# Kernel optimization log

Hardware: AMD Instinct MI355X
Metric: run time of the kernel (lower is better)

## Reference

```python
import jax, jax.numpy as jnp
import numpy as np

K = 3
Q = 4
NSF = 16
C2 = NSF * 2  # 32 channels in each multi-scale volume


def _x_shift():
    # Faithful replication of the torch init (note Python floor division: -3//2 == -2)
    grid = np.linspace(-K // 2, K // 2, K)  # [-2.0, -0.5, 1.0]
    g3 = np.stack(np.meshgrid(grid, grid, grid), axis=0).transpose(2, 1, 3, 0)
    return jnp.asarray(g3.reshape(-1, 3), dtype=jnp.float32)  # [27, 3]


def trilinear_sample(vol, coords):
    # vol: [C, D, H, W]; coords: [P, 3], normalized order (x->W, y->H, z->D)
    # matches F.grid_sample(mode='bilinear', padding_mode='border', align_corners=True)
    C, D, H, W = vol.shape
    def to_pix(c, size):
        return jnp.clip((c + 1.0) * 0.5 * (size - 1), 0.0, float(size - 1))
    ix = to_pix(coords[:, 0], W)
    iy = to_pix(coords[:, 1], H)
    iz = to_pix(coords[:, 2], D)
    x0f, y0f, z0f = jnp.floor(ix), jnp.floor(iy), jnp.floor(iz)
    x0 = x0f.astype(jnp.int32); y0 = y0f.astype(jnp.int32); z0 = z0f.astype(jnp.int32)
    x1 = jnp.minimum(x0 + 1, W - 1)
    y1 = jnp.minimum(y0 + 1, H - 1)
    z1 = jnp.minimum(z0 + 1, D - 1)
    fx, fy, fz = ix - x0f, iy - y0f, iz - z0f
    def g(zi, yi, xi):
        return vol[:, zi, yi, xi]  # [C, P]
    out = (g(z0, y0, x0) * ((1 - fz) * (1 - fy) * (1 - fx))
         + g(z0, y0, x1) * ((1 - fz) * (1 - fy) * fx)
         + g(z0, y1, x0) * ((1 - fz) * fy * (1 - fx))
         + g(z0, y1, x1) * ((1 - fz) * fy * fx)
         + g(z1, y0, x0) * (fz * (1 - fy) * (1 - fx))
         + g(z1, y0, x1) * (fz * (1 - fy) * fx)
         + g(z1, y1, x0) * (fz * fy * (1 - fx))
         + g(z1, y1, x1) * (fz * fy * fx))
    return out  # [C, P]


def _leaky(a):
    return jnp.where(a >= 0, a, 0.2 * a)


def reference(t, x, vol0, vol1, vol2, vol3, conv_w, conv_b, lfc_w, lfc_b,
              fc1_w, fc1_b, fc2_w, fc2_b, fc3_w, fc3_b, fc4_w, fc4_b):
    vols = [vol0, vol1, vol2, vol3]
    D1, D2, D3 = vol0.shape[2], vol0.shape[3], vol0.shape[4]
    Dm = max(D1, D2, D3)
    rescale = jnp.array([D3 / Dm, D2 / Dm, D1 / Dm], dtype=x.dtype)
    xs = _x_shift()
    m = x.shape[1]
    pts = x[0]  # [m, 3]
    cubes = jnp.zeros((C2, m * K * K * K), dtype=x.dtype)
    for q in range(Q):
        xq = pts[:, None, :] + xs * (2.0 * (2 ** q) / Dm)  # [m, 27, 3]
        xq = (xq / rescale).reshape(-1, 3)                  # [m*27, 3]
        cubes = cubes + trilinear_sample(vols[q][0], xq)    # sum over scales
    # torch wraps sampling in no_grad
    cubes = jax.lax.stop_gradient(cubes)
    # (C2, m, 27) -> (m, C2*27), matching view/permute/view in torch
    cubes = cubes.reshape(C2, m, K * K * K).transpose(1, 0, 2).reshape(m, C2 * K * K * K)
    # conv3d with kernel == cube -> per-point GEMM
    z_local = cubes @ conv_w.reshape(conv_w.shape[0], -1).T + conv_b   # [m, 64]
    z_local = z_local @ lfc_w.T + lfc_b                                 # [m, 128]
    z_point = _leaky(pts @ fc1_w.T + fc1_b)                             # [m, 128]
    z = jnp.concatenate([z_point, z_local], axis=-1)                    # [m, 256]
    z = _leaky(z @ fc2_w.T + fc2_b)                                     # [m, 512]
    z = _leaky(z @ fc3_w.T + fc3_b)                                     # [m, 256]
    dx = z @ fc4_w.T + fc4_b                                            # [m, 3]
    return dx[None]  # [1, m, 3]


def setup_inputs() -> dict:
    key = jax.random.key(0)
    ks = jax.random.split(key, 24)
    m, Dv, s = 50000, 64, 0.05
    inp = {
        't': jax.random.uniform(ks[0], (1,), dtype=jnp.float32),
        'x': jax.random.uniform(ks[1], (1, m, 3), dtype=jnp.float32),
    }
    for q in range(Q):
        inp[f'vol{q}'] = jax.random.normal(ks[2 + q], (1, C2, Dv, Dv, Dv), dtype=jnp.float32)
    inp['conv_w'] = jax.random.normal(ks[6], (NSF * 4, C2, K, K, K), dtype=jnp.float32) * s
    inp['conv_b'] = jax.random.normal(ks[7], (NSF * 4,), dtype=jnp.float32) * s
    inp['lfc_w'] = jax.random.normal(ks[8], (NSF * 8, NSF * 4), dtype=jnp.float32) * s
    inp['lfc_b'] = jax.random.normal(ks[9], (NSF * 8,), dtype=jnp.float32) * s
    inp['fc1_w'] = jax.random.normal(ks[10], (NSF * 8, 3), dtype=jnp.float32) * s
    inp['fc1_b'] = jax.random.normal(ks[11], (NSF * 8,), dtype=jnp.float32) * s
    inp['fc2_w'] = jax.random.normal(ks[12], (NSF * 32, NSF * 16), dtype=jnp.float32) * s
    inp['fc2_b'] = jax.random.normal(ks[13], (NSF * 32,), dtype=jnp.float32) * s
    inp['fc3_w'] = jax.random.normal(ks[14], (NSF * 16, NSF * 32), dtype=jnp.float32) * s
    inp['fc3_b'] = jax.random.normal(ks[15], (NSF * 16,), dtype=jnp.float32) * s
    inp['fc4_w'] = jax.random.normal(ks[16], (3, NSF * 16), dtype=jnp.float32) * s
    inp['fc4_b'] = jax.random.normal(ks[17], (3,), dtype=jnp.float32) * s
    return inp
```

## Files before the change

kernel.cpp:

```cpp
#include <hip/hip_runtime.h>
#include <hip/hip_bf16.h>

typedef __attribute__((ext_vector_type(8))) short short8;
typedef __attribute__((ext_vector_type(4))) float f32x4;
typedef __attribute__((ext_vector_type(2))) float f32x2;
typedef __attribute__((ext_vector_type(4))) int int32x4;

__device__ unsigned int llvm_amdgcn_raw_buffer_load_u32(int32x4 srsrc, int voffset,
                                                        int soffset, int aux)
    __asm("llvm.amdgcn.raw.buffer.load.i32");

#define VOXELS 262144
#define ZC_PAD 264
#define Z0_PAD 72
#define Z2_PAD 520
#define Z3_PAD 264
#define NCELL  512

template <bool VT16>
__global__ void k_transpose(const float* __restrict__ v0, const float* __restrict__ v1,
                            const float* __restrict__ v2, const float* __restrict__ v3,
                            void* __restrict__ vtp) {
    int b  = blockIdx.x;
    int q  = b >> 12;
    int zy = b & 4095;
    const float* src = (q == 0) ? v0 : (q == 1) ? v1 : (q == 2) ? v2 : v3;
    __shared__ float buf[32][65];
    int t = threadIdx.x;
    int x = t & 63, c0 = t >> 6;
    for (int cp = 0; cp < 32; cp += 4) {
        int c = c0 + cp;
        buf[c][x] = src[(size_t)c * VOXELS + (size_t)zy * 64 + x];
    }
    __syncthreads();
    int c = t & 31, xg = t >> 5;
    const size_t base = ((size_t)q * VOXELS + (size_t)zy * 64) * 32;
    for (int xx = xg; xx < 64; xx += 8) {
        if (VT16) ((__hip_bfloat16*)vtp)[base + xx * 32 + c] = __float2bfloat16(buf[c][xx]);
        else      ((float*)vtp)[base + xx * 32 + c] = buf[c][xx];
    }
}

__device__ __forceinline__ void prep_one(const float* __restrict__ W,
                                         __hip_bfloat16* __restrict__ wf,
                                         int K, int mode, int n) {
    int e = n & 7, lane = (n >> 3) & 63;
    int rest = n >> 9;
    int ksteps = K >> 5;
    int kstep = rest % ksteps, otile = rest / ksteps;
    int o = otile * 16 + (lane & 15);
    int k = kstep * 32 + (lane >> 4) * 8 + e;
    float v;
    if (mode == 1)      v = W[(size_t)o * K + (k & 31) * 27 + (k >> 5)];
    else if (mode == 2) v = (o < 3) ? W[(size_t)o * K + k] : 0.f;
    else                v = W[(size_t)o * K + k];
    wf[n] = __float2bfloat16(v);
}

__global__ void k_prepw_all(const float* __restrict__ conv_w, const float* __restrict__ lfc_w,
                            const float* __restrict__ fc2_w, const float* __restrict__ fc3_w,
                            const float* __restrict__ fc4_w,
                            __hip_bfloat16* __restrict__ w0f, __hip_bfloat16* __restrict__ w1f,
                            __hip_bfloat16* __restrict__ w2f, __hip_bfloat16* __restrict__ w3f,
                            __hip_bfloat16* __restrict__ w4f) {
    int n = blockIdx.x * blockDim.x + threadIdx.x;
    if (n < 55296)                prep_one(conv_w, w0f, 864, 1, n);
    else if (n < 63488)           prep_one(lfc_w,  w1f, 64,  0, n - 55296);
    else if (n < 194560)          prep_one(fc2_w,  w2f, 256, 0, n - 63488);
    else if (n < 325632)          prep_one(fc3_w,  w3f, 512, 0, n - 194560);
    else if (n < 329728)          prep_one(fc4_w,  w4f, 256, 2, n - 325632);
}

__device__ __forceinline__ int point_cell(float px, float py, float pz) {
    int cx = min(63, max(0, (int)(px * 31.5f + 31.5f))) >> 3;
    int cy = min(63, max(0, (int)(py * 31.5f + 31.5f))) >> 3;
    int cz = min(63, max(0, (int)(pz * 31.5f + 31.5f))) >> 3;
    int k = 0;
#pragma unroll
    for (int b = 0; b < 3; ++b)
        k |= (((cx >> b) & 1) << (3 * b)) | (((cy >> b) & 1) << (3 * b + 1))
           | (((cz >> b) & 1) << (3 * b + 2));
    return k;
}

__global__ void k_hist(const float* __restrict__ xin, int* __restrict__ hist, int m) {
    int p = blockIdx.x * blockDim.x + threadIdx.x;
    if (p >= m) return;
    atomicAdd(&hist[point_cell(xin[p * 3], xin[p * 3 + 1], xin[p * 3 + 2])], 1);
}

__global__ __launch_bounds__(64)
void k_scan(const int* __restrict__ hist, int* __restrict__ cursor) {
    const int t = threadIdx.x;
    int vals[8];
    int s = 0;
#pragma unroll
    for (int k = 0; k < 8; ++k) { vals[k] = hist[t * 8 + k]; s += vals[k]; }
    int pre = s;
#pragma unroll
    for (int off = 1; off < 64; off <<= 1) {
        int u = __shfl_up(pre, off);
        if (t >= off) pre += u;
    }
    int run = pre - s;
#pragma unroll
    for (int k = 0; k < 8; ++k) { cursor[t * 8 + k] = run; run += vals[k]; }
}

__global__ void k_scatter(const float* __restrict__ xin, int* __restrict__ cursor,
                          int* __restrict__ perm, int m) {
    int p = blockIdx.x * blockDim.x + threadIdx.x;
    if (p >= m) return;
    int cell = point_cell(xin[p * 3], xin[p * 3 + 1], xin[p * 3 + 2]);
    int pos = atomicAdd(&cursor[cell], 1);
    perm[pos] = p;
}

template <bool VT16, bool SORT>
__global__ __launch_bounds__(256, 4)
void k_sample(const float* __restrict__ xin, const void* __restrict__ vtp,
              const int* __restrict__ perm,
              __hip_bfloat16* __restrict__ fbuf, int m, int nblk) {
    __shared__ __align__(16) __hip_bfloat16 rowbuf[4][896];

    int b = blockIdx.x;
    {
        const int qd = nblk >> 3, r = nblk & 7;
        const int xcd = b & 7, i = b >> 3;
        b = (xcd < r) ? xcd * (qd + 1) + i : r * (qd + 1) + (xcd - r) * qd + i;
    }
    const int lane = threadIdx.x & 63;
    const int wv   = threadIdx.x >> 6;
    const int sp = b * 4 + wv;
    if (sp >= m) return;
    const int p = SORT ? perm[sp] : sp;

    const float px = xin[p * 3 + 0];
    const float py = xin[p * 3 + 1];
    const float pz = xin[p * 3 + 2];

    const int pr  = lane & 15;
    const int cxb = (lane >> 4) & 1;
    const int cyb = (lane >> 5) & 1;

    const float pxs = px * 31.5f + 31.5f;
    const float pys = py * 31.5f + 31.5f;
    const float pzs = pz * 31.5f + 31.5f;

    const int XS  = VT16 ? 6 : 7;
    const int YS  = VT16 ? 12 : 13;
    const int ZS  = VT16 ? 18 : 19;
    const int QS  = VT16 ? 24 : 25;
    const int PRB = VT16 ? 4 : 8;

    int   xoS[4][3], yoS[4][3], zoS[4][3], zdS[4][3];
    float wxS[4][3], wyS[4][3], wzS[4][3];
#pragma unroll
    for (int q = 0; q < 4; ++q) {
        const float sc31 = (float)(2 << q) * (31.5f / 64.0f);
#pragma unroll
        for (int pos = 0; pos < 3; ++pos) {
            const float gv = (-2.0f + 1.5f * (float)pos) * sc31;
            {
                float ix = fminf(fmaxf(pxs + gv, 0.f), 63.f);
                float xf = floorf(ix); int x0 = (int)xf; float fx = ix - xf;
                int x1 = min(x0 + 1, 63);
                xoS[q][pos] = ((cxb ? x1 : x0) << XS) + pr * PRB;
                wxS[q][pos] = cxb ? fx : 1.f - fx;
            }
            {
                float iy = fminf(fmaxf(pys + gv, 0.f), 63.f);
                float yf = floorf(iy); int y0 = (int)yf; float fy = iy - yf;
                int y1 = min(y0 + 1, 63);
                yoS[q][pos] = (cyb ? y1 : y0) << YS;
                wyS[q][pos] = cyb ? fy : 1.f - fy;
            }
            {
                float iz = fminf(fmaxf(pzs + gv, 0.f), 63.f);
                float zf = floorf(iz); int z0 = (int)zf; float fz = iz - zf;
                int z1 = min(z0 + 1, 63);
                zoS[q][pos] = (z0 << ZS) + (q << QS);
                zdS[q][pos] = (z1 - z0) << ZS;
                wzS[q][pos] = fz;
            }
        }
    }

    int32x4 srsrc;
    srsrc.x = (int)(unsigned)(uintptr_t)vtp;
    srsrc.y = (int)((uintptr_t)vtp >> 32);
    srsrc.z = -1;
    srsrc.w = 0x00020000;

    const char* __restrict__ vtb = (const char*)vtp;
#pragma unroll
    for (int j = 0; j < 3; ++j)
#pragma unroll
    for (int i = 0; i < 3; ++i) {
        int   yxo[4];
        float wyx[4];
#pragma unroll
        for (int q = 0; q < 4; ++q) {
            yxo[q] = yoS[q][i] + xoS[q][j];
            wyx[q] = wyS[q][i] * wxS[q][j];
        }
#pragma unroll
        for (int k = 0; k < 3; ++k) {
            f32x2 acc = {0.f, 0.f};
#pragma unroll
            for (int q = 0; q < 4; ++q) {
                const int a0 = zoS[q][k] + yxo[q];
                const int a1 = a0 + zdS[q][k];
                f32x2 r0, r1;
                if (VT16) {
                    const unsigned u0 = llvm_amdgcn_raw_buffer_load_u32(srsrc, a0, 0, 0);
                    const unsigned u1 = llvm_amdgcn_raw_buffer_load_u32(srsrc, a1, 0, 0);
                    r0.x = __uint_as_float(u0 << 16);
                    r0.y = __uint_as_float(u0 & 0xffff0000u);
                    r1.x = __uint_as_float(u1 << 16);
                    r1.y = __uint_as_float(u1 & 0xffff0000u);
                } else {
                    r0 = *(const f32x2*)(vtb + a0);
                    r1 = *(const f32x2*)(vtb + a1);
                }
                const float fz = wzS[q][k];
                const f32x2 fz2  = {fz, fz};
                const f32x2 wyx2 = {wyx[q], wyx[q]};
                const f32x2 t = r0 + (r1 - r0) * fz2;
                acc = acc + t * wyx2;
            }
            float ax = acc.x, ay = acc.y;
            ax += __shfl_xor(ax, 16); ax += __shfl_xor(ax, 32);
            ay += __shfl_xor(ay, 16); ay += __shfl_xor(ay, 32);
            if (lane < 16) {
                unsigned u;
                asm("v_cvt_pk_bf16_f32 %0, %1, %2" : "=v"(u) : "v"(ax), "v"(ay));
                ((unsigned*)&rowbuf[wv][0])[(j * 9 + i * 3 + k) * 16 + pr] = u;
            }
        }
    }

    {
        const f32x4* __restrict__ lsrc = (const f32x4*)&rowbuf[wv][0];
        f32x4* __restrict__ gdst = (f32x4*)(fbuf + (size_t)sp * 864);
#pragma unroll
        for (int r = 0; r < 2; ++r) {
            const int idx = r * 64 + lane;
            if (idx < 108) __builtin_nontemporal_store(lsrc[idx], &gdst[idx]);
        }
    }
}

template <bool SORT>
__global__ __launch_bounds__(512, 4)
void k_mlp(const float* __restrict__ xin, const __hip_bfloat16* __restrict__ fbuf,
           const int* __restrict__ perm,
           const __hip_bfloat16* __restrict__ w0f, const float* __restrict__ b0,
           const __hip_bfloat16* __restrict__ w1f, const float* __restrict__ b1,
           const float* __restrict__ fc1w, const float* __restrict__ fc1b,
           const __hip_bfloat16* __restrict__ w2f, const float* __restrict__ b2,
           const __hip_bfloat16* __restrict__ w3f, const float* __restrict__ b3,
           const __hip_bfloat16* __restrict__ w4f, const float* __restrict__ fc4b,
           float* __restrict__ out, int m) {
    __shared__ __align__(16) __hip_bfloat16 zcat[32][ZC_PAD];
    __shared__ __align__(16) __hip_bfloat16 z0l[32][Z0_PAD];
    __shared__ __align__(16) char shr[32 * 1744];
    __hip_bfloat16 (*rowA)[872]  = (__hip_bfloat16(*)[872])shr;
    __hip_bfloat16 (*z2l)[Z2_PAD] = (__hip_bfloat16(*)[Z2_PAD])shr;
    __hip_bfloat16 (*z3l)[Z3_PAD] = (__hip_bfloat16(*)[Z3_PAD])(shr + 33280);

    const int tid  = threadIdx.x;
    const int wave = tid >> 6;
    const int lane = tid & 63;
    const int p0   = blockIdx.x * 32;
    const int row  = lane & 15, g = lane >> 4;

    {
        const int rrow = (wave << 2) + (lane >> 4);
        const int srow = min(p0 + rrow, m - 1);
        const f32x4* __restrict__ src = (const f32x4*)(fbuf + (size_t)srow * 864);
        const int c16 = lane & 15;
#pragma unroll
        for (int k = 0; k < 7; ++k) {
            const int chunk = c16 + k * 16;
            if (chunk < 108)
                *(f32x4*)&rowA[rrow][chunk * 8] = src[chunk];
        }
    }

    {
        const int ptp = tid >> 4;
        const int og  = tid & 15;
        const int sp  = min(p0 + ptp, m - 1);
        const int p   = SORT ? perm[sp] : sp;
        const float qx = xin[p * 3 + 0], qy = xin[p * 3 + 1], qz = xin[p * 3 + 2];
#pragma unroll
        for (int r = 0; r < 8; ++r) {
            const int o = og * 8 + r;
            float v = qx * fc1w[o * 3 + 0] + qy * fc1w[o * 3 + 1] + qz * fc1w[o * 3 + 2] + fc1b[o];
            v = fmaxf(v, 0.2f * v);
            zcat[ptp][o] = __float2bfloat16(v);
        }
    }
    __syncthreads();

    {
        const int wc = wave & 3, wr = wave >> 2;
        f32x4 acc = {0.f, 0.f, 0.f, 0.f};
#pragma unroll
        for (int ks = 0; ks < 27; ++ks) {
            short8 af = *(const short8*)&rowA[wr * 16 + row][ks * 32 + g * 8];
            short8 bf = *(const short8*)(w0f + (((size_t)wc * 27 + ks) * 64 + lane) * 8);
            acc = __builtin_amdgcn_mfma_f32_16x16x32_bf16(af, bf, acc, 0, 0, 0);
        }
        const int o = wc * 16 + row;
        const float bias = b0[o];
#pragma unroll
        for (int r = 0; r < 4; ++r)
            z0l[wr * 16 + g * 4 + r][o] = __float2bfloat16(acc[r] + bias);
    }
    __syncthreads();

    {
        const int tc = wave;
        f32x4 acc0 = {0.f, 0.f, 0.f, 0.f}, acc1 = {0.f, 0.f, 0.f, 0.f};
#pragma unroll
        for (int ks = 0; ks < 2; ++ks) {
            short8 bf = *(const short8*)(w1f + (((size_t)tc * 2 + ks) * 64 + lane) * 8);
            short8 a0 = *(const short8*)&z0l[row][ks * 32 + g * 8];
            short8 a1 = *(const short8*)&z0l[16 + row][ks * 32 + g * 8];
            acc0 = __builtin_amdgcn_mfma_f32_16x16x32_bf16(a0, bf, acc0, 0, 0, 0);
            acc1 = __builtin_amdgcn_mfma_f32_16x16x32_bf16(a1, bf, acc1, 0, 0, 0);
        }
        const int o = tc * 16 + row;
        const float bias = b1[o];
#pragma unroll
        for (int r = 0; r < 4; ++r) {
            zcat[g * 4 + r][128 + o]      = __float2bfloat16(acc0[r] + bias);
            zcat[16 + g * 4 + r][128 + o] = __float2bfloat16(acc1[r] + bias);
        }
    }
    __syncthreads();

    {
        f32x4 acc[4][2];
#pragma unroll
        for (int c = 0; c < 4; ++c)
#pragma unroll
            for (int t = 0; t < 2; ++t) acc[c][t] = (f32x4){0.f, 0.f, 0.f, 0.f};
#pragma unroll
        for (int ks = 0; ks < 8; ++ks) {
            short8 a0 = *(const short8*)&zcat[row][ks * 32 + g * 8];
            short8 a1 = *(const short8*)&zcat[16 + row][ks * 32 + g * 8];
#pragma unroll
            for (int c = 0; c < 4; ++c) {
                short8 bf = *(const short8*)(w2f + (((size_t)(wave * 4 + c) * 8 + ks) * 64 + lane) * 8);
                acc[c][0] = __builtin_amdgcn_mfma_f32_16x16x32_bf16(a0, bf, acc[c][0], 0, 0, 0);
                acc[c][1] = __builtin_amdgcn_mfma_f32_16x16x32_bf16(a1, bf, acc[c][1], 0, 0, 0);
            }
        }
#pragma unroll
        for (int c = 0; c < 4; ++c) {
            const int o = (wave * 4 + c) * 16 + row;
            const float bias = b2[o];
#pragma unroll
            for (int r = 0; r < 4; ++r) {
                float v0 = acc[c][0][r] + bias; v0 = fmaxf(v0, 0.2f * v0);
                float v1 = acc[c][1][r] + bias; v1 = fmaxf(v1, 0.2f * v1);
                z2l[g * 4 + r][o]      = __float2bfloat16(v0);
                z2l[16 + g * 4 + r][o] = __float2bfloat16(v1);
            }
        }
    }
    __syncthreads();

    {
        f32x4 acc[2][2];
#pragma unroll
        for (int c = 0; c < 2; ++c)
#pragma unroll
            for (int t = 0; t < 2; ++t) acc[c][t] = (f32x4){0.f, 0.f, 0.f, 0.f};
#pragma unroll
        for (int ks = 0; ks < 16; ++ks) {
            short8 a0 = *(const short8*)&z2l[row][ks * 32 + g * 8];
            short8 a1 = *(const short8*)&z2l[16 + row][ks * 32 + g * 8];
#pragma unroll
            for (int c = 0; c < 2; ++c) {
                short8 bf = *(const short8*)(w3f + (((size_t)(wave * 2 + c) * 16 + ks) * 64 + lane) * 8);
                acc[c][0] = __builtin_amdgcn_mfma_f32_16x16x32_bf16(a0, bf, acc[c][0], 0, 0, 0);
                acc[c][1] = __builtin_amdgcn_mfma_f32_16x16x32_bf16(a1, bf, acc[c][1], 0, 0, 0);
            }
        }
#pragma unroll
        for (int c = 0; c < 2; ++c) {
            const int o = (wave * 2 + c) * 16 + row;
            const float bias = b3[o];
#pragma unroll
            for (int r = 0; r < 4; ++r) {
                float v0 = acc[c][0][r] + bias; v0 = fmaxf(v0, 0.2f * v0);
                float v1 = acc[c][1][r] + bias; v1 = fmaxf(v1, 0.2f * v1);
                z3l[g * 4 + r][o]      = __float2bfloat16(v0);
                z3l[16 + g * 4 + r][o] = __float2bfloat16(v1);
            }
        }
    }
    __syncthreads();

    if (wave < 2) {
        f32x4 acc = {0.f, 0.f, 0.f, 0.f};
#pragma unroll
        for (int ks = 0; ks < 8; ++ks) {
            short8 af = *(const short8*)&z3l[wave * 16 + row][ks * 32 + g * 8];
            short8 bf = *(const short8*)(w4f + (((size_t)ks) * 64 + lane) * 8);
            acc = __builtin_amdgcn_mfma_f32_16x16x32_bf16(af, bf, acc, 0, 0, 0);
        }
        const int o = row;
        if (o < 3) {
            const float bias = fc4b[o];
#pragma unroll
            for (int r = 0; r < 4; ++r) {
                const int spg = p0 + wave * 16 + g * 4 + r;
                if (spg < m) {
                    const int pg = SORT ? perm[spg] : spg;
                    out[pg * 3 + o] = acc[r] + bias;
                }
            }
        }
    }
}

extern "C" void kernel_launch(void* const* d_in, const int* in_sizes, int n_in,
                              void* d_out, int out_size, void* d_ws, size_t ws_size,
                              hipStream_t stream) {
    const float* x      = (const float*)d_in[1];
    const float* v0     = (const float*)d_in[2];
    const float* v1     = (const float*)d_in[3];
    const float* v2     = (const float*)d_in[4];
    const float* v3     = (const float*)d_in[5];
    const float* conv_w = (const float*)d_in[6];
    const float* conv_b = (const float*)d_in[7];
    const float* lfc_w  = (const float*)d_in[8];
    const float* lfc_b  = (const float*)d_in[9];
    const float* fc1_w  = (const float*)d_in[10];
    const float* fc1_b  = (const float*)d_in[11];
    const float* fc2_w  = (const float*)d_in[12];
    const float* fc2_b  = (const float*)d_in[13];
    const float* fc3_w  = (const float*)d_in[14];
    const float* fc3_b  = (const float*)d_in[15];
    const float* fc4_w  = (const float*)d_in[16];
    const float* fc4_b  = (const float*)d_in[17];
    float* out = (float*)d_out;
    const int m = in_sizes[1] / 3;

    char* ws = (char*)d_ws;
    size_t woff = 0;
    __hip_bfloat16* w0f = (__hip_bfloat16*)(ws + woff); woff += (size_t)55296 * 2;
    __hip_bfloat16* w1f = (__hip_bfloat16*)(ws + woff); woff += (size_t)8192 * 2;
    __hip_bfloat16* w2f = (__hip_bfloat16*)(ws + woff); woff += (size_t)131072 * 2;
    __hip_bfloat16* w3f = (__hip_bfloat16*)(ws + woff); woff += (size_t)131072 * 2;
    __hip_bfloat16* w4f = (__hip_bfloat16*)(ws + woff); woff += (size_t)4096 * 2;
    woff = (woff + 255) & ~(size_t)255;
    int* hist   = (int*)(ws + woff); woff += NCELL * 4;
    int* cursor = (int*)(ws + woff); woff += NCELL * 4;
    int* perm   = (int*)(ws + woff); woff += ((size_t)m * 4 + 255) & ~(size_t)255;

    const size_t vt32_bytes = (size_t)4 * VOXELS * 32 * 4;
    const size_t vt16_bytes = (size_t)4 * VOXELS * 32 * 2;
    const size_t fbytes     = ((size_t)m * 864 * 2 + 255) & ~(size_t)255;

    const size_t need_split16 = woff + vt16_bytes + fbytes;
    const size_t need_split32 = woff + vt32_bytes + fbytes;

    k_prepw_all<<<(329728 + 255) / 256, 256, 0, stream>>>(conv_w, lfc_w, fc2_w, fc3_w, fc4_w,
                                                          w0f, w1f, w2f, w3f, w4f);

    const int nsb = (m + 3) / 4;
    const int nb  = (m + 31) / 32;
    const int npb = (m + 255) / 256;

    if (ws_size >= need_split16) {
        void* vt = (void*)(ws + woff);
        __hip_bfloat16* fbuf = (__hip_bfloat16*)(ws + woff + vt16_bytes);
        hipMemsetAsync(hist, 0, NCELL * 4, stream);
        k_hist<<<npb, 256, 0, stream>>>(x, hist, m);
        k_scan<<<1, 64, 0, stream>>>(hist, cursor);
        k_scatter<<<npb, 256, 0, stream>>>(x, cursor, perm, m);
        k_transpose<true><<<16384, 256, 0, stream>>>(v0, v1, v2, v3, vt);
        k_sample<true, true><<<nsb, 256, 0, stream>>>(x, vt, perm, fbuf, m, nsb);
        k_mlp<true><<<nb, 512, 0, stream>>>(x, fbuf, perm, w0f, conv_b, w1f, lfc_b,
                                            fc1_w, fc1_b, w2f, fc2_b, w3f, fc3_b,
                                            w4f, fc4_b, out, m);
    } else if (ws_size >= need_split32) {
        void* vt = (void*)(ws + woff);
        __hip_bfloat16* fbuf = (__hip_bfloat16*)(ws + woff + vt32_bytes);
        hipMemsetAsync(hist, 0, NCELL * 4, stream);
        k_hist<<<npb, 256, 0, stream>>>(x, hist, m);
        k_scan<<<1, 64, 0, stream>>>(hist, cursor);
        k_scatter<<<npb, 256, 0, stream>>>(x, cursor, perm, m);
        k_transpose<false><<<16384, 256, 0, stream>>>(v0, v1, v2, v3, vt);
        k_sample<false, true><<<nsb, 256, 0, stream>>>(x, vt, perm, fbuf, m, nsb);
        k_mlp<true><<<nb, 512, 0, stream>>>(x, fbuf, perm, w0f, conv_b, w1f, lfc_b,
                                            fc1_w, fc1_b, w2f, fc2_b, w3f, fc3_b,
                                            w4f, fc4_b, out, m);
    } else {
        __hip_bfloat16* fbuf = (__hip_bfloat16*)(ws + woff);
        k_sample<false, false><<<nsb, 256, 0, stream>>>(x, nullptr, perm, fbuf, m, nsb);
        k_mlp<false><<<nb, 512, 0, stream>>>(x, fbuf, perm, w0f, conv_b, w1f, lfc_b,
                                             fc1_w, fc1_b, w2f, fc2_b, w3f, fc3_b,
                                             w4f, fc4_b, out, m);
    }
}
```

Before: 435.4 us.

## Fuse trilinear sampling into the MLP kernel with 1024-thread blocks

Merges the sampling kernel and the MLP kernel into one kernel, so each 32-point block gathers its 27x32 features straight into shared memory instead of writing them to a global bf16 buffer and reading them back. Block size rises to 1024 threads (16 waves), and the MLP stages' wave-to-tile mapping is reworked to match. An extra barrier inside the fc2 stage guards the shared buffer that is reused. This removes the global feature round trip and one launch, but adds register pressure under the new launch bounds and makes gather latency and MLP compute share the same blocks. The fallback path now always assumes the bf16 volume fits in workspace, and an empty branch remains.

```diff
diff --git a/kernel.cpp b/kernel.cpp
--- a/kernel.cpp
+++ b/kernel.cpp
@@ -15,6 +15,7 @@
 #define Z0_PAD 72
 #define Z2_PAD 520
 #define Z3_PAD 264
+#define RA_PAD 872
 #define NCELL  512
 
 template <bool VT16>
@@ -117,143 +118,8 @@
 }
 
 template <bool VT16, bool SORT>
-__global__ __launch_bounds__(256, 4)
-void k_sample(const float* __restrict__ xin, const void* __restrict__ vtp,
-              const int* __restrict__ perm,
-              __hip_bfloat16* __restrict__ fbuf, int m, int nblk) {
-    __shared__ __align__(16) __hip_bfloat16 rowbuf[4][896];
-
-    int b = blockIdx.x;
-    {
-        const int qd = nblk >> 3, r = nblk & 7;
-        const int xcd = b & 7, i = b >> 3;
-        b = (xcd < r) ? xcd * (qd + 1) + i : r * (qd + 1) + (xcd - r) * qd + i;
-    }
-    const int lane = threadIdx.x & 63;
-    const int wv   = threadIdx.x >> 6;
-    const int sp = b * 4 + wv;
-    if (sp >= m) return;
-    const int p = SORT ? perm[sp] : sp;
-
-    const float px = xin[p * 3 + 0];
-    const float py = xin[p * 3 + 1];
-    const float pz = xin[p * 3 + 2];
-
-    const int pr  = lane & 15;
-    const int cxb = (lane >> 4) & 1;
-    const int cyb = (lane >> 5) & 1;
-
-    const float pxs = px * 31.5f + 31.5f;
-    const float pys = py * 31.5f + 31.5f;
-    const float pzs = pz * 31.5f + 31.5f;
-
-    const int XS  = VT16 ? 6 : 7;
-    const int YS  = VT16 ? 12 : 13;
-    const int ZS  = VT16 ? 18 : 19;
-    const int QS  = VT16 ? 24 : 25;
-    const int PRB = VT16 ? 4 : 8;
-
-    int   xoS[4][3], yoS[4][3], zoS[4][3], zdS[4][3];
-    float wxS[4][3], wyS[4][3], wzS[4][3];
-#pragma unroll
-    for (int q = 0; q < 4; ++q) {
-        const float sc31 = (float)(2 << q) * (31.5f / 64.0f);
-#pragma unroll
-        for (int pos = 0; pos < 3; ++pos) {
-            const float gv = (-2.0f + 1.5f * (float)pos) * sc31;
-            {
-                float ix = fminf(fmaxf(pxs + gv, 0.f), 63.f);
-                float xf = floorf(ix); int x0 = (int)xf; float fx = ix - xf;
-                int x1 = min(x0 + 1, 63);
-                xoS[q][pos] = ((cxb ? x1 : x0) << XS) + pr * PRB;
-                wxS[q][pos] = cxb ? fx : 1.f - fx;
-            }
-            {
-                float iy = fminf(fmaxf(pys + gv, 0.f), 63.f);
-                float yf = floorf(iy); int y0 = (int)yf; float fy = iy - yf;
-                int y1 = min(y0 + 1, 63);
-                yoS[q][pos] = (cyb ? y1 : y0) << YS;
-                wyS[q][pos] = cyb ? fy : 1.f - fy;
-            }
-            {
-                float iz = fminf(fmaxf(pzs + gv, 0.f), 63.f);
-                float zf = floorf(iz); int z0 = (int)zf; float fz = iz - zf;
-                int z1 = min(z0 + 1, 63);
-                zoS[q][pos] = (z0 << ZS) + (q << QS);
-                zdS[q][pos] = (z1 - z0) << ZS;
-                wzS[q][pos] = fz;
-            }
-        }
-    }
-
-    int32x4 srsrc;
-    srsrc.x = (int)(unsigned)(uintptr_t)vtp;
-    srsrc.y = (int)((uintptr_t)vtp >> 32);
-    srsrc.z = -1;
-    srsrc.w = 0x00020000;
-
-    const char* __restrict__ vtb = (const char*)vtp;
-#pragma unroll
-    for (int j = 0; j < 3; ++j)
-#pragma unroll
-    for (int i = 0; i < 3; ++i) {
-        int   yxo[4];
-        float wyx[4];
-#pragma unroll
-        for (int q = 0; q < 4; ++q) {
-            yxo[q] = yoS[q][i] + xoS[q][j];
-            wyx[q] = wyS[q][i] * wxS[q][j];
-        }
-#pragma unroll
-        for (int k = 0; k < 3; ++k) {
-            f32x2 acc = {0.f, 0.f};
-#pragma unroll
-            for (int q = 0; q < 4; ++q) {
-                const int a0 = zoS[q][k] + yxo[q];
-                const int a1 = a0 + zdS[q][k];
-                f32x2 r0, r1;
-                if (VT16) {
-                    const unsigned u0 = llvm_amdgcn_raw_buffer_load_u32(srsrc, a0, 0, 0);
-                    const unsigned u1 = llvm_amdgcn_raw_buffer_load_u32(srsrc, a1, 0, 0);
-                    r0.x = __uint_as_float(u0 << 16);
-                    r0.y = __uint_as_float(u0 & 0xffff0000u);
-                    r1.x = __uint_as_float(u1 << 16);
-                    r1.y = __uint_as_float(u1 & 0xffff0000u);
-                } else {
-                    r0 = *(const f32x2*)(vtb + a0);
-                    r1 = *(const f32x2*)(vtb + a1);
-                }
-                const float fz = wzS[q][k];
-                const f32x2 fz2  = {fz, fz};
-                const f32x2 wyx2 = {wyx[q], wyx[q]};
-                const f32x2 t = r0 + (r1 - r0) * fz2;
-                acc = acc + t * wyx2;
-            }
-            float ax = acc.x, ay = acc.y;
-            ax += __shfl_xor(ax, 16); ax += __shfl_xor(ax, 32);
-            ay += __shfl_xor(ay, 16); ay += __shfl_xor(ay, 32);
-            if (lane < 16) {
-                unsigned u;
-                asm("v_cvt_pk_bf16_f32 %0, %1, %2" : "=v"(u) : "v"(ax), "v"(ay));
-                ((unsigned*)&rowbuf[wv][0])[(j * 9 + i * 3 + k) * 16 + pr] = u;
-            }
-        }
-    }
-
-    {
-        const f32x4* __restrict__ lsrc = (const f32x4*)&rowbuf[wv][0];
-        f32x4* __restrict__ gdst = (f32x4*)(fbuf + (size_t)sp * 864);
-#pragma unroll
-        for (int r = 0; r < 2; ++r) {
-            const int idx = r * 64 + lane;
-            if (idx < 108) __builtin_nontemporal_store(lsrc[idx], &gdst[idx]);
-        }
-    }
-}
-
-template <bool SORT>
-__global__ __launch_bounds__(512, 4)
-void k_mlp(const float* __restrict__ xin, const __hip_bfloat16* __restrict__ fbuf,
+__global__ __launch_bounds__(1024, 8)
+void k_all(const float* __restrict__ xin, const void* __restrict__ vtp,
            const int* __restrict__ perm,
            const __hip_bfloat16* __restrict__ w0f, const float* __restrict__ b0,
            const __hip_bfloat16* __restrict__ w1f, const float* __restrict__ b1,
@@ -261,42 +127,148 @@
            const __hip_bfloat16* __restrict__ w2f, const float* __restrict__ b2,
            const __hip_bfloat16* __restrict__ w3f, const float* __restrict__ b3,
            const __hip_bfloat16* __restrict__ w4f, const float* __restrict__ fc4b,
-           float* __restrict__ out, int m) {
+           float* __restrict__ out, int m, int nblk) {
     __shared__ __align__(16) __hip_bfloat16 zcat[32][ZC_PAD];
     __shared__ __align__(16) __hip_bfloat16 z0l[32][Z0_PAD];
     __shared__ __align__(16) char shr[32 * 1744];
-    __hip_bfloat16 (*rowA)[872]  = (__hip_bfloat16(*)[872])shr;
-    __hip_bfloat16 (*z2l)[Z2_PAD] = (__hip_bfloat16(*)[Z2_PAD])shr;
-    __hip_bfloat16 (*z3l)[Z3_PAD] = (__hip_bfloat16(*)[Z3_PAD])(shr + 33280);
-
+    __hip_bfloat16 (*rowA)[RA_PAD]  = (__hip_bfloat16(*)[RA_PAD])shr;
+    __hip_bfloat16 (*z2l)[Z2_PAD]   = (__hip_bfloat16(*)[Z2_PAD])shr;
+    __hip_bfloat16 (*z3l)[Z3_PAD]   = (__hip_bfloat16(*)[Z3_PAD])(shr + 33280);
+
+    int b = blockIdx.x;
+    {
+        const int qd = nblk >> 3, r = nblk & 7;
+        const int xcd = b & 7, i = b >> 3;
+        b = (xcd < r) ? xcd * (qd + 1) + i : r * (qd + 1) + (xcd - r) * qd + i;
+    }
     const int tid  = threadIdx.x;
     const int wave = tid >> 6;
     const int lane = tid & 63;
-    const int p0   = blockIdx.x * 32;
+    const int p0   = b * 32;
     const int row  = lane & 15, g = lane >> 4;
 
     {
-        const int rrow = (wave << 2) + (lane >> 4);
-        const int srow = min(p0 + rrow, m - 1);
-        const f32x4* __restrict__ src = (const f32x4*)(fbuf + (size_t)srow * 864);
-        const int c16 = lane & 15;
-#pragma unroll
-        for (int k = 0; k < 7; ++k) {
-            const int chunk = c16 + k * 16;
-            if (chunk < 108)
-                *(f32x4*)&rowA[rrow][chunk * 8] = src[chunk];
-        }
-    }
-
-    {
-        const int ptp = tid >> 4;
-        const int og  = tid & 15;
+        const int pr  = lane & 15;
+        const int cxb = (lane >> 4) & 1;
+        const int cyb = (lane >> 5) & 1;
+
+        const int XS  = VT16 ? 6 : 7;
+        const int YS  = VT16 ? 12 : 13;
+        const int ZS  = VT16 ? 18 : 19;
+        const int QS  = VT16 ? 24 : 25;
+        const int PRB = VT16 ? 4 : 8;
+
+        int32x4 srsrc;
+        srsrc.x = (int)(unsigned)(uintptr_t)vtp;
+        srsrc.y = (int)((uintptr_t)vtp >> 32);
+        srsrc.z = -1;
+        srsrc.w = 0x00020000;
+        const char* __restrict__ vtb = (const char*)vtp;
+
+#pragma unroll 1
+        for (int rep = 0; rep < 2; ++rep) {
+            const int pt = wave + rep * 16;
+            const int sp = min(p0 + pt, m - 1);
+            const int p  = SORT ? perm[sp] : sp;
+
+            const float px = xin[p * 3 + 0];
+            const float py = xin[p * 3 + 1];
+            const float pz = xin[p * 3 + 2];
+            const float pxs = px * 31.5f + 31.5f;
+            const float pys = py * 31.5f + 31.5f;
+            const float pzs = pz * 31.5f + 31.5f;
+
+            int   xoS[4][3], yoS[4][3], zoS[4][3], zdS[4][3];
+            float wxS[4][3], wyS[4][3], wzS[4][3];
+#pragma unroll
+            for (int q = 0; q < 4; ++q) {
+                const float sc31 = (float)(2 << q) * (31.5f / 64.0f);
+#pragma unroll
+                for (int pos = 0; pos < 3; ++pos) {
+                    const float gv = (-2.0f + 1.5f * (float)pos) * sc31;
+                    {
+                        float ix = fminf(fmaxf(pxs + gv, 0.f), 63.f);
+                        float xf = floorf(ix); int x0 = (int)xf; float fx = ix - xf;
+                        int x1 = min(x0 + 1, 63);
+                        xoS[q][pos] = ((cxb ? x1 : x0) << XS) + pr * PRB;
+                        wxS[q][pos] = cxb ? fx : 1.f - fx;
+                    }
+                    {
+                        float iy = fminf(fmaxf(pys + gv, 0.f), 63.f);
+                        float yf = floorf(iy); int y0 = (int)yf; float fy = iy - yf;
+                        int y1 = min(y0 + 1, 63);
+                        yoS[q][pos] = (cyb ? y1 : y0) << YS;
+                        wyS[q][pos] = cyb ? fy : 1.f - fy;
+                    }
+                    {
+                        float iz = fminf(fmaxf(pzs + gv, 0.f), 63.f);
+                        float zf = floorf(iz); int z0 = (int)zf; float fz = iz - zf;
+                        int z1 = min(z0 + 1, 63);
+                        zoS[q][pos] = (z0 << ZS) + (q << QS);
+                        zdS[q][pos] = (z1 - z0) << ZS;
+                        wzS[q][pos] = fz;
+                    }
+                }
+            }
+
+#pragma unroll
+            for (int j = 0; j < 3; ++j)
+#pragma unroll
+            for (int i = 0; i < 3; ++i) {
+                int   yxo[4];
+                float wyx[4];
+#pragma unroll
+                for (int q = 0; q < 4; ++q) {
+                    yxo[q] = yoS[q][i] + xoS[q][j];
+                    wyx[q] = wyS[q][i] * wxS[q][j];
+                }
+#pragma unroll
+                for (int k = 0; k < 3; ++k) {
+                    f32x2 acc = {0.f, 0.f};
+#pragma unroll
+                    for (int q = 0; q < 4; ++q) {
+                        const int a0 = zoS[q][k] + yxo[q];
+                        const int a1 = a0 + zdS[q][k];
+                        f32x2 r0, r1;
+                        if (VT16) {
+                            const unsigned u0 = llvm_amdgcn_raw_buffer_load_u32(srsrc, a0, 0, 0);
+                            const unsigned u1 = llvm_amdgcn_raw_buffer_load_u32(srsrc, a1, 0, 0);
+                            r0.x = __uint_as_float(u0 << 16);
+                            r0.y = __uint_as_float(u0 & 0xffff0000u);
+                            r1.x = __uint_as_float(u1 << 16);
+                            r1.y = __uint_as_float(u1 & 0xffff0000u);
+                        } else {
+                            r0 = *(const f32x2*)(vtb + a0);
+                            r1 = *(const f32x2*)(vtb + a1);
+                        }
+                        const float fz = wzS[q][k];
+                        const f32x2 fz2  = {fz, fz};
+                        const f32x2 wyx2 = {wyx[q], wyx[q]};
+                        const f32x2 t = r0 + (r1 - r0) * fz2;
+                        acc = acc + t * wyx2;
+                    }
+                    float ax = acc.x, ay = acc.y;
+                    ax += __shfl_xor(ax, 16); ax += __shfl_xor(ax, 32);
+                    ay += __shfl_xor(ay, 16); ay += __shfl_xor(ay, 32);
+                    if (lane < 16) {
+                        unsigned u;
+                        asm("v_cvt_pk_bf16_f32 %0, %1, %2" : "=v"(u) : "v"(ax), "v"(ay));
+                        ((unsigned*)&rowA[pt][0])[(j * 9 + i * 3 + k) * 16 + pr] = u;
+                    }
+                }
+            }
+        }
+    }
+
+    {
+        const int ptp = tid >> 5;
+        const int og  = tid & 31;
         const int sp  = min(p0 + ptp, m - 1);
         const int p   = SORT ? perm[sp] : sp;
         const float qx = xin[p * 3 + 0], qy = xin[p * 3 + 1], qz = xin[p * 3 + 2];
 #pragma unroll
-        for (int r = 0; r < 8; ++r) {
-            const int o = og * 8 + r;
+        for (int r = 0; r < 4; ++r) {
+            const int o = og + 32 * r;
             float v = qx * fc1w[o * 3 + 0] + qy * fc1w[o * 3 + 1] + qz * fc1w[o * 3 + 2] + fc1b[o];
             v = fmaxf(v, 0.2f * v);
             zcat[ptp][o] = __float2bfloat16(v);
@@ -304,7 +276,7 @@
     }
     __syncthreads();
 
-    {
+    if (wave < 8) {
         const int wc = wave & 3, wr = wave >> 2;
         f32x4 acc = {0.f, 0.f, 0.f, 0.f};
 #pragma unroll
@@ -322,30 +294,26 @@
     __syncthreads();
 
     {
-        const int tc = wave;
-        f32x4 acc0 = {0.f, 0.f, 0.f, 0.f}, acc1 = {0.f, 0.f, 0.f, 0.f};
+        const int tr = wave >> 3, tc = wave & 7;
+        f32x4 acc = {0.f, 0.f, 0.f, 0.f};
 #pragma unroll
         for (int ks = 0; ks < 2; ++ks) {
+            short8 af = *(const short8*)&z0l[tr * 16 + row][ks * 32 + g * 8];
             short8 bf = *(const short8*)(w1f + (((size_t)tc * 2 + ks) * 64 + lane) * 8);
-            short8 a0 = *(const short8*)&z0l[row][ks * 32 + g * 8];
-            short8 a1 = *(const short8*)&z0l[16 + row][ks * 32 + g * 8];
-            acc0 = __builtin_amdgcn_mfma_f32_16x16x32_bf16(a0, bf, acc0, 0, 0, 0);
-            acc1 = __builtin_amdgcn_mfma_f32_16x16x32_bf16(a1, bf, acc1, 0, 0, 0);
+            acc = __builtin_amdgcn_mfma_f32_16x16x32_bf16(af, bf, acc, 0, 0, 0);
         }
         const int o = tc * 16 + row;
         const float bias = b1[o];
 #pragma unroll
-        for (int r = 0; r < 4; ++r) {
-            zcat[g * 4 + r][128 + o]      = __float2bfloat16(acc0[r] + bias);
-            zcat[16 + g * 4 + r][128 + o] = __float2bfloat16(acc1[r] + bias);
-        }
-    }
-    __syncthreads();
-
-    {
-        f32x4 acc[4][2];
-#pragma unroll
-        for (int c = 0; c < 4; ++c)
+        for (int r = 0; r < 4; ++r)
+            zcat[tr * 16 + g * 4 + r][128 + o] = __float2bfloat16(acc[r] + bias);
+    }
+    __syncthreads();
+
+    {
+        f32x4 acc[2][2];
+#pragma unroll
+        for (int c = 0; c < 2; ++c)
 #pragma unroll
             for (int t = 0; t < 2; ++t) acc[c][t] = (f32x4){0.f, 0.f, 0.f, 0.f};
 #pragma unroll
@@ -353,15 +321,16 @@
             short8 a0 = *(const short8*)&zcat[row][ks * 32 + g * 8];
             short8 a1 = *(const short8*)&zcat[16 + row][ks * 32 + g * 8];
 #pragma unroll
-            for (int c = 0; c < 4; ++c) {
-                short8 bf = *(const short8*)(w2f + (((size_t)(wave * 4 + c) * 8 + ks) * 64 + lane) * 8);
+            for (int c = 0; c < 2; ++c) {
+                short8 bf = *(const short8*)(w2f + (((size_t)(wave * 2 + c) * 8 + ks) * 64 + lane) * 8);
                 acc[c][0] = __builtin_amdgcn_mfma_f32_16x16x32_bf16(a0, bf, acc[c][0], 0, 0, 0);
                 acc[c][1] = __builtin_amdgcn_mfma_f32_16x16x32_bf16(a1, bf, acc[c][1], 0, 0, 0);
             }
         }
-#pragma unroll
-        for (int c = 0; c < 4; ++c) {
-            const int o = (wave * 4 + c) * 16 + row;
+        __syncthreads();
+#pragma unroll
+        for (int c = 0; c < 2; ++c) {
+            const int o = (wave * 2 + c) * 16 + row;
             const float bias = b2[o];
 #pragma unroll
             for (int r = 0; r < 4; ++r) {
@@ -375,33 +344,23 @@
     __syncthreads();
 
     {
-        f32x4 acc[2][2];
-#pragma unroll
-        for (int c = 0; c < 2; ++c)
-#pragma unroll
-            for (int t = 0; t < 2; ++t) acc[c][t] = (f32x4){0.f, 0.f, 0.f, 0.f};
+        f32x4 acc0 = {0.f, 0.f, 0.f, 0.f}, acc1 = {0.f, 0.f, 0.f, 0.f};
 #pragma unroll
         for (int ks = 0; ks < 16; ++ks) {
             short8 a0 = *(const short8*)&z2l[row][ks * 32 + g * 8];
             short8 a1 = *(const short8*)&z2l[16 + row][ks * 32 + g * 8];
-#pragma unroll
-            for (int c = 0; c < 2; ++c) {
-                short8 bf = *(const short8*)(w3f + (((size_t)(wave * 2 + c) * 16 + ks) * 64 + lane) * 8);
-                acc[c][0] = __builtin_amdgcn_mfma_f32_16x16x32_bf16(a0, bf, acc[c][0], 0, 0, 0);
-                acc[c][1] = __builtin_amdgcn_mfma_f32_16x16x32_bf16(a1, bf, acc[c][1], 0, 0, 0);
-            }
-        }
-#pragma unroll
-        for (int c = 0; c < 2; ++c) {
-            const int o = (wave * 2 + c) * 16 + row;
-            const float bias = b3[o];
-#pragma unroll
-            for (int r = 0; r < 4; ++r) {
-                float v0 = acc[c][0][r] + bias; v0 = fmaxf(v0, 0.2f * v0);
-                float v1 = acc[c][1][r] + bias; v1 = fmaxf(v1, 0.2f * v1);
-                z3l[g * 4 + r][o]      = __float2bfloat16(v0);
-                z3l[16 + g * 4 + r][o] = __float2bfloat16(v1);
-            }
+            short8 bf = *(const short8*)(w3f + (((size_t)wave * 16 + ks) * 64 + lane) * 8);
+            acc0 = __builtin_amdgcn_mfma_f32_16x16x32_bf16(a0, bf, acc0, 0, 0, 0);
+            acc1 = __builtin_amdgcn_mfma_f32_16x16x32_bf16(a1, bf, acc1, 0, 0, 0);
+        }
+        const int o = wave * 16 + row;
+        const float bias = b3[o];
+#pragma unroll
+        for (int r = 0; r < 4; ++r) {
+            float v0 = acc0[r] + bias; v0 = fmaxf(v0, 0.2f * v0);
+            float v1 = acc1[r] + bias; v1 = fmaxf(v1, 0.2f * v1);
+            z3l[g * 4 + r][o]      = __float2bfloat16(v0);
+            z3l[16 + g * 4 + r][o] = __float2bfloat16(v1);
         }
     }
     __syncthreads();
@@ -466,47 +425,33 @@
 
     const size_t vt32_bytes = (size_t)4 * VOXELS * 32 * 4;
     const size_t vt16_bytes = (size_t)4 * VOXELS * 32 * 2;
-    const size_t fbytes     = ((size_t)m * 864 * 2 + 255) & ~(size_t)255;
-
-    const size_t need_split16 = woff + vt16_bytes + fbytes;
-    const size_t need_split32 = woff + vt32_bytes + fbytes;
+
+    const size_t need16 = woff + vt16_bytes;
+    const size_t need32 = woff + vt32_bytes;
 
     k_prepw_all<<<(329728 + 255) / 256, 256, 0, stream>>>(conv_w, lfc_w, fc2_w, fc3_w, fc4_w,
                                                           w0f, w1f, w2f, w3f, w4f);
 
-    const int nsb = (m + 3) / 4;
     const int nb  = (m + 31) / 32;
     const int npb = (m + 255) / 256;
 
-    if (ws_size >= need_split16) {
+    if (ws_size >= need16) {
         void* vt = (void*)(ws + woff);
-        __hip_bfloat16* fbuf = (__hip_bfloat16*)(ws + woff + vt16_bytes);
         hipMemsetAsync(hist, 0, NCELL * 4, stream);
         k_hist<<<npb, 256, 0, stream>>>(x, hist, m);
         k_scan<<<1, 64, 0, stream>>>(hist, cursor);
         k_scatter<<<npb, 256, 0, stream>>>(x, cursor, perm, m);
+        if (ws_size >= need32) {
+        }
         k_transpose<true><<<16384, 256, 0, stream>>>(v0, v1, v2, v3, vt);
-        k_sample<true, true><<<nsb, 256, 0, stream>>>(x, vt, perm, fbuf, m, nsb);
-        k_mlp<true><<<nb, 512, 0, stream>>>(x, fbuf, perm, w0f, conv_b, w1f, lfc_b,
-                                            fc1_w, fc1_b, w2f, fc2_b, w3f, fc3_b,
-                                            w4f, fc4_b, out, m);
-    } else if (ws_size >= need_split32) {
+        k_all<true, true><<<nb, 1024, 0, stream>>>(x, vt, perm, w0f, conv_b, w1f, lfc_b,
+                                                   fc1_w, fc1_b, w2f, fc2_b, w3f, fc3_b,
+                                                   w4f, fc4_b, out, m, nb);
+    } else {
         void* vt = (void*)(ws + woff);
-        __hip_bfloat16* fbuf = (__hip_bfloat16*)(ws + woff + vt32_bytes);
-        hipMemsetAsync(hist, 0, NCELL * 4, stream);
-        k_hist<<<npb, 256, 0, stream>>>(x, hist, m);
-        k_scan<<<1, 64, 0, stream>>>(hist, cursor);
-        k_scatter<<<npb, 256, 0, stream>>>(x, cursor, perm, m);
-        k_transpose<false><<<16384, 256, 0, stream>>>(v0, v1, v2, v3, vt);
-        k_sample<false, true><<<nsb, 256, 0, stream>>>(x, vt, perm, fbuf, m, nsb);
-        k_mlp<true><<<nb, 512, 0, stream>>>(x, fbuf, perm, w0f, conv_b, w1f, lfc_b,
-                                            fc1_w, fc1_b, w2f, fc2_b, w3f, fc3_b,
-                                            w4f, fc4_b, out, m);
-    } else {
-        __hip_bfloat16* fbuf = (__hip_bfloat16*)(ws + woff);
-        k_sample<false, false><<<nsb, 256, 0, stream>>>(x, nullptr, perm, fbuf, m, nsb);
-        k_mlp<false><<<nb, 512, 0, stream>>>(x, fbuf, perm, w0f, conv_b, w1f, lfc_b,
-                                             fc1_w, fc1_b, w2f, fc2_b, w3f, fc3_b,
-                                             w4f, fc4_b, out, m);
-    }
-}
+        k_transpose<true><<<16384, 256, 0, stream>>>(v0, v1, v2, v3, vt);
+        k_all<true, false><<<nb, 1024, 0, stream>>>(x, vt, nullptr, w0f, conv_b, w1f, lfc_b,
+                                                    fc1_w, fc1_b, w2f, fc2_b, w3f, fc3_b,
+                                                    w4f, fc4_b, out, m, nb);
+    }
+}
```

New measurement: 833.2 us. 1.91x slower.
